# Kernel optimization log

Hardware: AMD Instinct MI355X
Metric: run time of the kernel (lower is better)

The kernel has to match this reference:

```python
import jax, jax.numpy as jnp
import numpy as np

NUM_SLOTS = 64
MEMORY_DIM = 512
EMBED_DIM = 1024
SCALE = MEMORY_DIM ** (-0.5)


def setup_inputs() -> dict:
    key = jax.random.key(0)
    ks = jax.random.split(key, 7)
    B, S, E, Dm = 8, 4096, EMBED_DIM, MEMORY_DIM
    s = 0.02
    return {
        "embeddings": jax.random.normal(ks[0], (B, S, E), dtype=jnp.float32),
        "W_write": jax.random.normal(ks[1], (E, Dm), dtype=jnp.float32) * s,
        "b_write": jnp.zeros((Dm,), dtype=jnp.float32),
        "W_query": jax.random.normal(ks[2], (E, Dm), dtype=jnp.float32) * s,
        "b_query": jnp.zeros((Dm,), dtype=jnp.float32),
        "W_out": jax.random.normal(ks[3], (Dm, E), dtype=jnp.float32) * s,
        "b_out": jnp.zeros((E,), dtype=jnp.float32),
    }


def reference(embeddings, W_write, b_write, W_query, b_query, W_out, b_out):
    B, S, E = embeddings.shape
    M, Dm = NUM_SLOTS, MEMORY_DIM
    # Precompute per-token projections (linear, so identical to per-step).
    write_vals = jnp.einsum('bse,ed->bsd', embeddings, W_write) + b_write  # [B,S,Dm]
    queries = jnp.einsum('bse,ed->bsd', embeddings, W_query) + b_query      # [B,S,Dm]
    addrs = jnp.arange(S) % M  # hash(position) = position % M

    def step(carry, xs):
        memory, written = carry            # [B,M,Dm], [B,M] bool
        q, wv, addr = xs                   # [B,Dm], [B,Dm], scalar int
        # read BEFORE write (current token not yet in memory)
        sim = jnp.einsum('bd,bmd->bm', q, memory) * SCALE
        sim = jnp.where(written, sim, -jnp.inf)
        attn = jax.nn.softmax(sim, axis=-1)
        attn = jnp.nan_to_num(attn)        # all-unwritten -> zeros
        retrieved = jnp.einsum('bm,bmd->bd', attn, memory)
        memory = memory.at[:, addr, :].set(wv)
        written = written.at[:, addr].set(True)
        return (memory, written), retrieved

    mem0 = jnp.zeros((B, M, Dm), dtype=embeddings.dtype)
    wr0 = jnp.zeros((B, M), dtype=bool)
    xs = (queries.transpose(1, 0, 2), write_vals.transpose(1, 0, 2), addrs)
    _, retrieved = jax.lax.scan(step, (mem0, wr0), xs)  # [S,B,Dm]
    retrieved = retrieved.transpose(1, 0, 2)            # [B,S,Dm]
    # read_out is linear per-step -> apply once over the whole sequence
    return jnp.einsum('bsd,de->bse', retrieved, W_out) + b_out
```

## Files before the change

kernel.cpp:

```cpp
#include <hip/hip_runtime.h>
#include <hip/hip_bf16.h>
#include <math.h>


#define BATCH   8
#define S_LEN   4096
#define EMB     1024
#define DM      512
#define MROWS   (BATCH * S_LEN)
#define SCALE_F 0.04419417382415922f

typedef __attribute__((ext_vector_type(4))) float f32x4;
typedef __attribute__((ext_vector_type(8))) short short8;

__device__ __forceinline__ unsigned short f2bf(float f) {
    __hip_bfloat16 h = __float2bfloat16(f);
    return *reinterpret_cast<unsigned short*>(&h);
}

__global__ __launch_bounds__(256) void prep(
    const float4* __restrict__ emb4, ushort4* __restrict__ embb4,
    const float* __restrict__ W_wr, const float* __restrict__ W_qr,
    const float* __restrict__ W_out,
    const float* __restrict__ b_wr, const float* __restrict__ b_qr,
    __hip_bfloat16* __restrict__ wcat, __hip_bfloat16* __restrict__ wout,
    float* __restrict__ bcat)
{
    const int bx = blockIdx.x;
    if (bx < 32768) {
        int id = bx * 256 + threadIdx.x;
        float4 v = emb4[id];
        ushort4 o;
        o.x = f2bf(v.x); o.y = f2bf(v.y); o.z = f2bf(v.z); o.w = f2bf(v.w);
        embb4[id] = o;
    } else if (bx < 32768 + 2048) {
        int id = (bx - 32768) * 256 + threadIdx.x;
        int n = id >> 10, k = id & 1023;
        wcat[id] = __float2bfloat16(W_wr[k * 512 + n]);
    } else if (bx < 32768 + 4096) {
        int id = (bx - 32768 - 2048) * 256 + threadIdx.x;
        int n = id >> 10, k = id & 1023;
        wcat[(size_t)DM * EMB + id] = __float2bfloat16(W_qr[k * 512 + n]);
    } else if (bx < 32768 + 6144) {
        int id = (bx - 32768 - 4096) * 256 + threadIdx.x;
        int n = id >> 9, k = id & 511;
        wout[id] = __float2bfloat16(W_out[k * 1024 + n]);
    } else {
        int i = threadIdx.x;
#pragma unroll
        for (int r = 0; r < 4; ++r, i += 256)
            bcat[i] = (i < 512) ? b_wr[i] : b_qr[i - 512];
    }
}

template<bool BF16OUT, bool TRANSLO>
__global__ __launch_bounds__(512, 2) void gemm256(
    const __hip_bfloat16* __restrict__ A, int lda,
    const __hip_bfloat16* __restrict__ Bt, int ldb,
    const float* __restrict__ bias,
    void* __restrict__ Cv, int ldc,
    __hip_bfloat16* __restrict__ wvtp,
    int K, int nbx)
{
    __shared__ __align__(16) char smem[131072];

    const int nwg = gridDim.x;
    const int bid = blockIdx.x;
    const int cpx = nwg >> 3;
    const int swz = (bid & 7) * cpx + (bid >> 3);
    const int bm0 = (swz / nbx) << 8;
    const int bn0 = (swz % nbx) << 8;

    const int tid  = threadIdx.x;
    const int lane = tid & 63;
    const int w    = tid >> 6;
    const int wm   = w >> 2, wn = w & 3;
    const int l15  = lane & 15, lhi = lane >> 4;
    const int nt   = K >> 6;

    const int r64 = tid >> 3;
    const int cg8 = ((tid & 7) ^ (r64 & 7)) << 3;

    auto stageA = [&](int buf, int kt, int r) {
        const __hip_bfloat16* g =
            A + (size_t)(bm0 + r * 64 + r64) * lda + kt + cg8;
        char* l = smem + buf * 65536 + r * 8192 + w * 1024;
        __builtin_amdgcn_global_load_lds(
            (const __attribute__((address_space(1))) unsigned int*)g,
            (__attribute__((address_space(3))) unsigned int*)l, 16, 0, 0);
    };
    auto stageB = [&](int buf, int kt, int r) {
        const __hip_bfloat16* g =
            Bt + (size_t)(bn0 + r * 64 + r64) * ldb + kt + cg8;
        char* l = smem + buf * 65536 + 32768 + r * 8192 + w * 1024;
        __builtin_amdgcn_global_load_lds(
            (const __attribute__((address_space(1))) unsigned int*)g,
            (__attribute__((address_space(3))) unsigned int*)l, 16, 0, 0);
    };

    f32x4 acc[8][4] = {};

    stageB(0, 0, 0); stageB(0, 0, 1); stageB(0, 0, 2); stageB(0, 0, 3);
    stageA(0, 0, 0); stageA(0, 0, 2); stageA(0, 0, 1); stageA(0, 0, 3);
    asm volatile("s_waitcnt vmcnt(2)" ::: "memory");
    __builtin_amdgcn_s_barrier();

    for (int t = 0; t < nt; ++t) {
        const int cur = t & 1;
        const bool pf = (t + 1 < nt);
        const int kt1 = (t + 1) << 6;
        const char* sA = smem + cur * 65536;
        const char* sB = sA + 32768;

        short8 af[4][2], b0[2][2], b1[2][2];

        if (pf) { stageB(cur ^ 1, kt1, 0); stageB(cur ^ 1, kt1, 1); }
#pragma unroll
        for (int ni = 0; ni < 2; ++ni) {
            const int r = wn * 64 + ni * 16 + l15;
#pragma unroll
            for (int kk = 0; kk < 2; ++kk) {
                const int pc = (kk * 4 + lhi) ^ (r & 7);
                b0[ni][kk] = *(const short8*)(sB + r * 128 + (pc << 4));
            }
        }
#pragma unroll
        for (int mi = 0; mi < 4; ++mi) {
            const int r = wm * 128 + mi * 16 + l15;
#pragma unroll
            for (int kk = 0; kk < 2; ++kk) {
                const int pc = (kk * 4 + lhi) ^ (r & 7);
                af[mi][kk] = *(const short8*)(sA + r * 128 + (pc << 4));
            }
        }
        __builtin_amdgcn_s_setprio(1);
#pragma unroll
        for (int mi = 0; mi < 4; ++mi)
#pragma unroll
            for (int ni = 0; ni < 2; ++ni)
#pragma unroll
                for (int kk = 0; kk < 2; ++kk)
                    acc[mi][ni] = __builtin_amdgcn_mfma_f32_16x16x32_bf16(
                        af[mi][kk], b0[ni][kk], acc[mi][ni], 0, 0, 0);
        __builtin_amdgcn_s_setprio(0);

        if (pf) { stageB(cur ^ 1, kt1, 2); stageB(cur ^ 1, kt1, 3); }
#pragma unroll
        for (int ni = 0; ni < 2; ++ni) {
            const int r = wn * 64 + 32 + ni * 16 + l15;
#pragma unroll
            for (int kk = 0; kk < 2; ++kk) {
                const int pc = (kk * 4 + lhi) ^ (r & 7);
                b1[ni][kk] = *(const short8*)(sB + r * 128 + (pc << 4));
            }
        }
        __builtin_amdgcn_s_setprio(1);
#pragma unroll
        for (int mi = 0; mi < 4; ++mi)
#pragma unroll
            for (int ni = 0; ni < 2; ++ni)
#pragma unroll
                for (int kk = 0; kk < 2; ++kk)
                    acc[mi][2 + ni] = __builtin_amdgcn_mfma_f32_16x16x32_bf16(
                        af[mi][kk], b1[ni][kk], acc[mi][2 + ni], 0, 0, 0);
        __builtin_amdgcn_s_setprio(0);

        if (pf) { asm volatile("s_waitcnt vmcnt(4)" ::: "memory"); }
        else    { asm volatile("s_waitcnt vmcnt(0)" ::: "memory"); }
        __builtin_amdgcn_s_barrier();

        if (pf) { stageA(cur ^ 1, kt1, 0); stageA(cur ^ 1, kt1, 2); }
#pragma unroll
        for (int mi = 0; mi < 4; ++mi) {
            const int r = wm * 128 + 64 + mi * 16 + l15;
#pragma unroll
            for (int kk = 0; kk < 2; ++kk) {
                const int pc = (kk * 4 + lhi) ^ (r & 7);
                af[mi][kk] = *(const short8*)(sA + r * 128 + (pc << 4));
            }
        }
        __builtin_amdgcn_s_setprio(1);
#pragma unroll
        for (int mi = 0; mi < 4; ++mi)
#pragma unroll
            for (int ni = 0; ni < 2; ++ni)
#pragma unroll
                for (int kk = 0; kk < 2; ++kk)
                    acc[4 + mi][ni] = __builtin_amdgcn_mfma_f32_16x16x32_bf16(
                        af[mi][kk], b0[ni][kk], acc[4 + mi][ni], 0, 0, 0);
        __builtin_amdgcn_s_setprio(0);

        if (pf) { stageA(cur ^ 1, kt1, 1); stageA(cur ^ 1, kt1, 3); }
        __builtin_amdgcn_s_setprio(1);
#pragma unroll
        for (int mi = 0; mi < 4; ++mi)
#pragma unroll
            for (int ni = 0; ni < 2; ++ni)
#pragma unroll
                for (int kk = 0; kk < 2; ++kk)
                    acc[4 + mi][2 + ni] = __builtin_amdgcn_mfma_f32_16x16x32_bf16(
                        af[mi][kk], b1[ni][kk], acc[4 + mi][2 + ni], 0, 0, 0);
        __builtin_amdgcn_s_setprio(0);

        asm volatile("s_waitcnt vmcnt(2)" ::: "memory");
        __builtin_amdgcn_s_barrier();
    }

    float bv[4];
#pragma unroll
    for (int N = 0; N < 4; ++N)
        bv[N] = bias[bn0 + wn * 64 + (N >> 1) * 32 + (N & 1) * 16 + l15];

#pragma unroll
    for (int M = 0; M < 8; ++M) {
        const int row = bm0 + wm * 128 + (M >> 2) * 64 + (M & 3) * 16 + lhi * 4;
#pragma unroll
        for (int N = 0; N < 4; ++N) {
            const int col = bn0 + wn * 64 + (N >> 1) * 32 + (N & 1) * 16 + l15;
            float v[4];
#pragma unroll
            for (int reg = 0; reg < 4; ++reg)
                v[reg] = acc[M][N][reg] + bv[N];

#pragma unroll
            for (int reg = 0; reg < 4; ++reg) {
                if (BF16OUT)
                    ((__hip_bfloat16*)Cv)[(size_t)(row + reg) * ldc + col] =
                        __float2bfloat16(v[reg]);
                else
                    ((float*)Cv)[(size_t)(row + reg) * ldc + col] = v[reg];
            }
            if (TRANSLO && col < 512) {
                union { unsigned short s[4]; uint2 u; } tv;
#pragma unroll
                for (int reg = 0; reg < 4; ++reg) tv.s[reg] = f2bf(v[reg]);
                *(uint2*)((unsigned short*)wvtp
                          + (((size_t)((row >> 12) * 512 + col)) << 12)
                          + (row & 4095)) = tv.u;
            }
        }
    }
}

__global__ __launch_bounds__(256) void attn_mfma(
    const __hip_bfloat16* __restrict__ WVQ,
    const __hip_bfloat16* __restrict__ WVT,
    __hip_bfloat16* __restrict__ R)
{
    __shared__ __align__(16) unsigned short p_lds[64][136];

    const int blk0 = blockIdx.x;
    const int blk  = (blk0 & 7) * 64 + (blk0 >> 3);
    const int b   = blk >> 6;
    const int t0  = (blk & 63) << 6;
    const int jmin = (t0 == 0) ? 64 : 0;
    const size_t bbase = (size_t)b << 12;
    const int tid  = threadIdx.x;
    const int lane = tid & 63;
    const int w    = tid >> 6;
    const int l15  = lane & 15;
    const int lhi  = lane >> 4;

    f32x4 acc[8] = {};
    const __hip_bfloat16* q0 =
        WVQ + ((bbase + t0 + w * 16 + l15) << 10) + 512 + lhi * 8;

    const __hip_bfloat16* brow[8];
#pragma unroll
    for (int nt = 0; nt < 8; ++nt) {
        int aj = t0 - 64 + nt * 16 + l15;
        if (aj < 0) aj = 0;
        brow[nt] = WVQ + ((bbase + aj) << 10) + lhi * 8;
    }

#pragma unroll 2
    for (int kt = 0; kt < 16; ++kt) {
        short8 qa = *(const short8*)(q0 + kt * 32);
#pragma unroll
        for (int nt = 0; nt < 8; ++nt) {
            short8 bv = *(const short8*)(brow[nt] + kt * 32);
            acc[nt] = __builtin_amdgcn_mfma_f32_16x16x32_bf16(qa, bv, acc[nt], 0, 0, 0);
        }
    }

    float m4[4] = { -1e30f, -1e30f, -1e30f, -1e30f };
#pragma unroll
    for (int nt = 0; nt < 8; ++nt)
#pragma unroll
        for (int reg = 0; reg < 4; ++reg) {
            int i = w * 16 + lhi * 4 + reg;
            int j = nt * 16 + l15;
            bool valid = (j >= i) && (j <= i + 63) && (j >= jmin);
            float s = valid ? acc[nt][reg] * SCALE_F : -1e30f;
            acc[nt][reg] = s;
            m4[reg] = fmaxf(m4[reg], s);
        }
#pragma unroll
    for (int off = 8; off >= 1; off >>= 1)
#pragma unroll
        for (int reg = 0; reg < 4; ++reg)
            m4[reg] = fmaxf(m4[reg], __shfl_xor(m4[reg], off, 64));

    float sum4[4] = {};
#pragma unroll
    for (int nt = 0; nt < 8; ++nt)
#pragma unroll
        for (int reg = 0; reg < 4; ++reg) {
            float s = acc[nt][reg];
            float p = (s > -1e29f) ? __expf(s - m4[reg]) : 0.f;
            acc[nt][reg] = p;
            sum4[reg] += p;
        }
#pragma unroll
    for (int off = 8; off >= 1; off >>= 1)
#pragma unroll
        for (int reg = 0; reg < 4; ++reg)
            sum4[reg] += __shfl_xor(sum4[reg], off, 64);

    float rs4[4];
#pragma unroll
    for (int reg = 0; reg < 4; ++reg)
        rs4[reg] = (sum4[reg] > 0.f) ? 1.f / sum4[reg] : 0.f;

#pragma unroll
    for (int nt = 0; nt < 8; ++nt)
#pragma unroll
        for (int reg = 0; reg < 4; ++reg)
            p_lds[w * 16 + lhi * 4 + reg][nt * 16 + l15] =
                f2bf(acc[nt][reg] * rs4[reg]);

    __syncthreads();

    short8 pa[4];
#pragma unroll
    for (int kt = 0; kt < 4; ++kt)
        pa[kt] = *(const short8*)&p_lds[w * 16 + l15][kt * 32 + lhi * 8];

    int tclamp[4];
#pragma unroll
    for (int kt = 0; kt < 4; ++kt) {
        int ti = t0 - 64 + kt * 32 + lhi * 8;
        tclamp[kt] = ti < 0 ? 0 : ti;
    }

    const size_t vbase = (size_t)b * 512;
#pragma unroll 2
    for (int nt = 0; nt < 32; ++nt) {
        int d = nt * 16 + l15;
        f32x4 a = {};
#pragma unroll
        for (int kt = 0; kt < 4; ++kt) {
            short8 bv = *(const short8*)(WVT + ((vbase + d) << 12) + tclamp[kt]);
            a = __builtin_amdgcn_mfma_f32_16x16x32_bf16(pa[kt], bv, a, 0, 0, 0);
        }
        size_t rb = (bbase + t0 + w * 16 + lhi * 4) << 9;
#pragma unroll
        for (int reg = 0; reg < 4; ++reg)
            R[rb + ((size_t)reg << 9) + d] = __float2bfloat16(a[reg]);
    }
}

extern "C" void kernel_launch(void* const* d_in, const int* in_sizes, int n_in,
                              void* d_out, int out_size, void* d_ws, size_t ws_size,
                              hipStream_t stream)
{
    const float* emb   = (const float*)d_in[0];
    const float* W_wr  = (const float*)d_in[1];
    const float* b_wr  = (const float*)d_in[2];
    const float* W_qr  = (const float*)d_in[3];
    const float* b_qr  = (const float*)d_in[4];
    const float* W_out = (const float*)d_in[5];
    const float* b_out = (const float*)d_in[6];
    float* out = (float*)d_out;

    char* ws = (char*)d_ws;
    __hip_bfloat16* embb = (__hip_bfloat16*)(ws);
    __hip_bfloat16* rbuf = (__hip_bfloat16*)(ws);
    __hip_bfloat16* wvq  = (__hip_bfloat16*)(ws + (((size_t)64) << 20));
    __hip_bfloat16* wvt  = (__hip_bfloat16*)(ws + (((size_t)128) << 20));
    __hip_bfloat16* wcat = (__hip_bfloat16*)(ws + (((size_t)160) << 20));
    __hip_bfloat16* wout = (__hip_bfloat16*)(ws + (((size_t)162) << 20));
    float*          bcat = (float*)        (ws + (((size_t)163) << 20));

    prep<<<dim3(38913), dim3(256), 0, stream>>>(
        (const float4*)emb, (ushort4*)embb,
        W_wr, W_qr, W_out, b_wr, b_qr, wcat, wout, bcat);

    gemm256<true, true><<<dim3(512), dim3(512), 0, stream>>>(
        embb, EMB, wcat, EMB, bcat, (void*)wvq, 1024, wvt, EMB, 4);

    attn_mfma<<<dim3(MROWS / 64), dim3(256), 0, stream>>>(wvq, wvt, rbuf);

    gemm256<false, false><<<dim3(512), dim3(512), 0, stream>>>(
        rbuf, DM, wout, DM, b_out, (void*)out, EMB, nullptr, DM, 4);
}
```

Baseline: 240.4 us.

## Shrink attention tile to 32 queries and resynchronize GEMM pipeline barriers

The attention kernel now handles 32 query rows per block with 128 threads, so each block covers a 96-key window (6 tiles) instead of 128 keys (8 tiles). This cuts wasted QK and PV MFMA work on masked keys and doubles the block count. The GEMM main loop moves its waitcnt and barriers so that each LDS half-stage gets its own barrier around the prefetch issues. That adds more barriers per iteration and may change whether the LDS double buffer stays race-free.

```diff
diff --git a/kernel.cpp b/kernel.cpp
--- a/kernel.cpp
+++ b/kernel.cpp
@@ -54,7 +54,7 @@
 }
 
 template<bool BF16OUT, bool TRANSLO>
-__global__ __launch_bounds__(512, 2) void gemm256(
+__global__ __launch_bounds__(512, 2) void gemm_k64(
     const __hip_bfloat16* __restrict__ A, int lda,
     const __hip_bfloat16* __restrict__ Bt, int ldb,
     const float* __restrict__ bias,
@@ -102,8 +102,6 @@
 
     stageB(0, 0, 0); stageB(0, 0, 1); stageB(0, 0, 2); stageB(0, 0, 3);
     stageA(0, 0, 0); stageA(0, 0, 2); stageA(0, 0, 1); stageA(0, 0, 3);
-    asm volatile("s_waitcnt vmcnt(2)" ::: "memory");
-    __builtin_amdgcn_s_barrier();
 
     for (int t = 0; t < nt; ++t) {
         const int cur = t & 1;
@@ -112,9 +110,11 @@
         const char* sA = smem + cur * 65536;
         const char* sB = sA + 32768;
 
-        short8 af[4][2], b0[2][2], b1[2][2];
-
+        short8 aF[4][2], b0[2][2], b1[2][2];
+
+        asm volatile("s_waitcnt vmcnt(2)" ::: "memory");
         if (pf) { stageB(cur ^ 1, kt1, 0); stageB(cur ^ 1, kt1, 1); }
+        asm volatile("s_barrier" ::: "memory");
 #pragma unroll
         for (int ni = 0; ni < 2; ++ni) {
             const int r = wn * 64 + ni * 16 + l15;
@@ -130,7 +130,7 @@
 #pragma unroll
             for (int kk = 0; kk < 2; ++kk) {
                 const int pc = (kk * 4 + lhi) ^ (r & 7);
-                af[mi][kk] = *(const short8*)(sA + r * 128 + (pc << 4));
+                aF[mi][kk] = *(const short8*)(sA + r * 128 + (pc << 4));
             }
         }
         __builtin_amdgcn_s_setprio(1);
@@ -141,10 +141,11 @@
 #pragma unroll
                 for (int kk = 0; kk < 2; ++kk)
                     acc[mi][ni] = __builtin_amdgcn_mfma_f32_16x16x32_bf16(
-                        af[mi][kk], b0[ni][kk], acc[mi][ni], 0, 0, 0);
+                        aF[mi][kk], b0[ni][kk], acc[mi][ni], 0, 0, 0);
         __builtin_amdgcn_s_setprio(0);
 
         if (pf) { stageB(cur ^ 1, kt1, 2); stageB(cur ^ 1, kt1, 3); }
+        asm volatile("s_barrier" ::: "memory");
 #pragma unroll
         for (int ni = 0; ni < 2; ++ni) {
             const int r = wn * 64 + 32 + ni * 16 + l15;
@@ -162,21 +163,23 @@
 #pragma unroll
                 for (int kk = 0; kk < 2; ++kk)
                     acc[mi][2 + ni] = __builtin_amdgcn_mfma_f32_16x16x32_bf16(
-                        af[mi][kk], b1[ni][kk], acc[mi][2 + ni], 0, 0, 0);
+                        aF[mi][kk], b1[ni][kk], acc[mi][2 + ni], 0, 0, 0);
         __builtin_amdgcn_s_setprio(0);
 
-        if (pf) { asm volatile("s_waitcnt vmcnt(4)" ::: "memory"); }
-        else    { asm volatile("s_waitcnt vmcnt(0)" ::: "memory"); }
-        __builtin_amdgcn_s_barrier();
-
-        if (pf) { stageA(cur ^ 1, kt1, 0); stageA(cur ^ 1, kt1, 2); }
+        if (pf) {
+            asm volatile("s_waitcnt vmcnt(4)" ::: "memory");
+            stageA(cur ^ 1, kt1, 0); stageA(cur ^ 1, kt1, 2);
+        } else {
+            asm volatile("s_waitcnt vmcnt(0)" ::: "memory");
+        }
+        asm volatile("s_barrier" ::: "memory");
 #pragma unroll
         for (int mi = 0; mi < 4; ++mi) {
             const int r = wm * 128 + 64 + mi * 16 + l15;
 #pragma unroll
             for (int kk = 0; kk < 2; ++kk) {
                 const int pc = (kk * 4 + lhi) ^ (r & 7);
-                af[mi][kk] = *(const short8*)(sA + r * 128 + (pc << 4));
+                aF[mi][kk] = *(const short8*)(sA + r * 128 + (pc << 4));
             }
         }
         __builtin_amdgcn_s_setprio(1);
@@ -187,10 +190,11 @@
 #pragma unroll
                 for (int kk = 0; kk < 2; ++kk)
                     acc[4 + mi][ni] = __builtin_amdgcn_mfma_f32_16x16x32_bf16(
-                        af[mi][kk], b0[ni][kk], acc[4 + mi][ni], 0, 0, 0);
+                        aF[mi][kk], b0[ni][kk], acc[4 + mi][ni], 0, 0, 0);
         __builtin_amdgcn_s_setprio(0);
 
         if (pf) { stageA(cur ^ 1, kt1, 1); stageA(cur ^ 1, kt1, 3); }
+        asm volatile("s_barrier" ::: "memory");
         __builtin_amdgcn_s_setprio(1);
 #pragma unroll
         for (int mi = 0; mi < 4; ++mi)
@@ -199,11 +203,8 @@
 #pragma unroll
                 for (int kk = 0; kk < 2; ++kk)
                     acc[4 + mi][2 + ni] = __builtin_amdgcn_mfma_f32_16x16x32_bf16(
-                        af[mi][kk], b1[ni][kk], acc[4 + mi][2 + ni], 0, 0, 0);
+                        aF[mi][kk], b1[ni][kk], acc[4 + mi][2 + ni], 0, 0, 0);
         __builtin_amdgcn_s_setprio(0);
-
-        asm volatile("s_waitcnt vmcnt(2)" ::: "memory");
-        __builtin_amdgcn_s_barrier();
     }
 
     float bv[4];
@@ -242,18 +243,18 @@
     }
 }
 
-__global__ __launch_bounds__(256) void attn_mfma(
+__global__ __launch_bounds__(128) void attn_mfma32(
     const __hip_bfloat16* __restrict__ WVQ,
     const __hip_bfloat16* __restrict__ WVT,
     __hip_bfloat16* __restrict__ R)
 {
-    __shared__ __align__(16) unsigned short p_lds[64][136];
+    __shared__ __align__(16) unsigned short p_lds[32][104];
 
     const int blk0 = blockIdx.x;
-    const int blk  = (blk0 & 7) * 64 + (blk0 >> 3);
-    const int b   = blk >> 6;
-    const int t0  = (blk & 63) << 6;
-    const int jmin = (t0 == 0) ? 64 : 0;
+    const int blk  = (blk0 & 7) * 128 + (blk0 >> 3);
+    const int b   = blk >> 7;
+    const int t0  = (blk & 127) << 5;
+    const int jmin = (t0 >= 64) ? 0 : 64 - t0;
     const size_t bbase = (size_t)b << 12;
     const int tid  = threadIdx.x;
     const int lane = tid & 63;
@@ -261,13 +262,13 @@
     const int l15  = lane & 15;
     const int lhi  = lane >> 4;
 
-    f32x4 acc[8] = {};
+    f32x4 acc[6] = {};
     const __hip_bfloat16* q0 =
         WVQ + ((bbase + t0 + w * 16 + l15) << 10) + 512 + lhi * 8;
 
-    const __hip_bfloat16* brow[8];
-#pragma unroll
-    for (int nt = 0; nt < 8; ++nt) {
+    const __hip_bfloat16* brow[6];
+#pragma unroll
+    for (int nt = 0; nt < 6; ++nt) {
         int aj = t0 - 64 + nt * 16 + l15;
         if (aj < 0) aj = 0;
         brow[nt] = WVQ + ((bbase + aj) << 10) + lhi * 8;
@@ -277,7 +278,7 @@
     for (int kt = 0; kt < 16; ++kt) {
         short8 qa = *(const short8*)(q0 + kt * 32);
 #pragma unroll
-        for (int nt = 0; nt < 8; ++nt) {
+        for (int nt = 0; nt < 6; ++nt) {
             short8 bv = *(const short8*)(brow[nt] + kt * 32);
             acc[nt] = __builtin_amdgcn_mfma_f32_16x16x32_bf16(qa, bv, acc[nt], 0, 0, 0);
         }
@@ -285,7 +286,7 @@
 
     float m4[4] = { -1e30f, -1e30f, -1e30f, -1e30f };
 #pragma unroll
-    for (int nt = 0; nt < 8; ++nt)
+    for (int nt = 0; nt < 6; ++nt)
 #pragma unroll
         for (int reg = 0; reg < 4; ++reg) {
             int i = w * 16 + lhi * 4 + reg;
@@ -303,7 +304,7 @@
 
     float sum4[4] = {};
 #pragma unroll
-    for (int nt = 0; nt < 8; ++nt)
+    for (int nt = 0; nt < 6; ++nt)
 #pragma unroll
         for (int reg = 0; reg < 4; ++reg) {
             float s = acc[nt][reg];
@@ -323,7 +324,7 @@
         rs4[reg] = (sum4[reg] > 0.f) ? 1.f / sum4[reg] : 0.f;
 
 #pragma unroll
-    for (int nt = 0; nt < 8; ++nt)
+    for (int nt = 0; nt < 6; ++nt)
 #pragma unroll
         for (int reg = 0; reg < 4; ++reg)
             p_lds[w * 16 + lhi * 4 + reg][nt * 16 + l15] =
@@ -331,14 +332,14 @@
 
     __syncthreads();
 
-    short8 pa[4];
-#pragma unroll
-    for (int kt = 0; kt < 4; ++kt)
+    short8 pa[3];
+#pragma unroll
+    for (int kt = 0; kt < 3; ++kt)
         pa[kt] = *(const short8*)&p_lds[w * 16 + l15][kt * 32 + lhi * 8];
 
-    int tclamp[4];
-#pragma unroll
-    for (int kt = 0; kt < 4; ++kt) {
+    int tclamp[3];
+#pragma unroll
+    for (int kt = 0; kt < 3; ++kt) {
         int ti = t0 - 64 + kt * 32 + lhi * 8;
         tclamp[kt] = ti < 0 ? 0 : ti;
     }
@@ -349,7 +350,7 @@
         int d = nt * 16 + l15;
         f32x4 a = {};
 #pragma unroll
-        for (int kt = 0; kt < 4; ++kt) {
+        for (int kt = 0; kt < 3; ++kt) {
             short8 bv = *(const short8*)(WVT + ((vbase + d) << 12) + tclamp[kt]);
             a = __builtin_amdgcn_mfma_f32_16x16x32_bf16(pa[kt], bv, a, 0, 0, 0);
         }
@@ -386,11 +387,11 @@
         (const float4*)emb, (ushort4*)embb,
         W_wr, W_qr, W_out, b_wr, b_qr, wcat, wout, bcat);
 
-    gemm256<true, true><<<dim3(512), dim3(512), 0, stream>>>(
+    gemm_k64<true, true><<<dim3(512), dim3(512), 0, stream>>>(
         embb, EMB, wcat, EMB, bcat, (void*)wvq, 1024, wvt, EMB, 4);
 
-    attn_mfma<<<dim3(MROWS / 64), dim3(256), 0, stream>>>(wvq, wvt, rbuf);
-
-    gemm256<false, false><<<dim3(512), dim3(512), 0, stream>>>(
+    attn_mfma32<<<dim3(MROWS / 32), dim3(128), 0, stream>>>(wvq, wvt, rbuf);
+
+    gemm_k64<false, false><<<dim3(512), dim3(512), 0, stream>>>(
         rbuf, DM, wout, DM, b_out, (void*)out, EMB, nullptr, DM, 4);
 }
```

After: 222.0 us. 1.08x faster.
